# Kernel tuning notes

Measured on AMD Instinct MI355X. Metric: run time of the kernel, lower is better.

## Reference

```python
import jax, jax.numpy as jnp
import numpy as np

B, T, DM = 4, 2048, 2048
H, HKV, D = 16, 4, 128
ROPE_BASE = 10000.0


def setup_inputs() -> dict:
    key = jax.random.key(0)
    ks = jax.random.split(key, 5)
    x = jax.random.normal(ks[0], (B, T, DM), dtype=jnp.float32)
    s = 1.0 / np.sqrt(DM)
    Wq = jax.random.normal(ks[1], (H * D, DM), dtype=jnp.float32) * s
    Wk = jax.random.normal(ks[2], (HKV * D, DM), dtype=jnp.float32) * s
    Wv = jax.random.normal(ks[3], (HKV * D, DM), dtype=jnp.float32) * s
    Wo = jax.random.normal(ks[4], (DM, H * D), dtype=jnp.float32) * (1.0 / np.sqrt(H * D))
    temp = jnp.ones((H,), dtype=jnp.float32) * np.sqrt(D)  # registered buffer (unused on fallback path)
    return {"x": x, "Wq": Wq, "Wk": Wk, "Wv": Wv, "Wo": Wo, "temp": temp, "curvature": 1}


def _rms_norm(x):
    # F.rms_norm with default eps = finfo(dtype).eps, no learnable weight
    eps = jnp.finfo(x.dtype).eps
    return x * jax.lax.rsqrt(jnp.mean(x * x, axis=-1, keepdims=True) + eps)


def _rope_cos_sin(t_len, d, dtype):
    inv_freq = 1.0 / (ROPE_BASE ** (jnp.arange(0, d, 2, dtype=jnp.float32) / d))
    freqs = jnp.outer(jnp.arange(t_len, dtype=jnp.float32), inv_freq)  # [T, D/2]
    cos = jnp.cos(freqs)[None, :, None, :].astype(dtype)
    sin = jnp.sin(freqs)[None, :, None, :].astype(dtype)
    return cos, sin


def _apply_rotary(x, cos, sin):
    d = x.shape[-1] // 2
    x1, x2 = x[..., :d], x[..., d:]
    return jnp.concatenate([x1 * cos + x2 * sin, -x1 * sin + x2 * cos], axis=-1)


def reference(x, Wq, Wk, Wv, Wo, temp, curvature):
    b, t, _ = x.shape
    q = (x @ Wq.T).reshape(b, t, H, D)
    k = (x @ Wk.T).reshape(b, t, HKV, D)
    v = (x @ Wv.T).reshape(b, t, HKV, D)
    q, k = _rms_norm(q), _rms_norm(k)
    cos, sin = _rope_cos_sin(t, D, q.dtype)
    q = _apply_rotary(q, cos, sin)
    k = _apply_rotary(k, cos, sin)
    rep = H // HKV
    k = jnp.repeat(k, rep, axis=2)  # [b, t, H, D] GQA expand
    v = jnp.repeat(v, rep, axis=2)
    scale = 1.0 / np.sqrt(D)
    scores = jnp.einsum('bqhd,bkhd->bhqk', q, k) * scale
    causal = jnp.tril(jnp.ones((t, t), dtype=bool))
    scores = jnp.where(causal[None, None], scores, jnp.finfo(scores.dtype).min)
    p = jax.nn.softmax(scores, axis=-1)
    attn = jnp.einsum('bhqk,bkhd->bqhd', p, v).reshape(b, t, H * D)
    out = attn @ Wo.T
    spatial_norm = jnp.zeros((1,), dtype=x.dtype)
    return out, spatial_norm
```

## Files before the change

kernel.cpp:

```cpp
#include <hip/hip_runtime.h>
#include <hip/hip_bf16.h>

typedef __attribute__((ext_vector_type(8))) short short8;
typedef __attribute__((ext_vector_type(4))) float f32x4;
using bf16 = __hip_bfloat16;

__device__ inline unsigned short f2bfu(float x) {
  bf16 h = __float2bfloat16(x);
  return __builtin_bit_cast(unsigned short, h);
}

__device__ __forceinline__ void gll16(const void* g, void* l) {
  __builtin_amdgcn_global_load_lds(
      (const __attribute__((address_space(1))) unsigned int*)g,
      (__attribute__((address_space(3))) unsigned int*)l, 16, 0, 0);
}

__global__ __launch_bounds__(256) void cast_f32_bf16(const float4* __restrict__ src,
                                                     unsigned long long* __restrict__ dst,
                                                     int n4) {
  int i = blockIdx.x * 256 + threadIdx.x;
  if (i >= n4) return;
  float4 v = src[i];
  unsigned long long r = (unsigned long long)f2bfu(v.x)
                       | ((unsigned long long)f2bfu(v.y) << 16)
                       | ((unsigned long long)f2bfu(v.z) << 32)
                       | ((unsigned long long)f2bfu(v.w) << 48);
  dst[i] = r;
}

__device__ inline void store_cvt(float* p, float v) { *p = v; }
__device__ inline void store_cvt(bf16* p, float v) { *p = __float2bfloat16(v); }

template <typename OutT>
__global__ __launch_bounds__(256) void gemm_bt(const bf16* __restrict__ A,
                                               const bf16* __restrict__ B,
                                               OutT* __restrict__ C,
                                               int M, int N, int K) {
  __shared__ __align__(16) bf16 As[128][32];
  __shared__ __align__(16) bf16 Bs[128][32];
  const int tid = threadIdx.x;
  const int wave = tid >> 6, lane = tid & 63;
  const int wm = wave >> 1, wn = wave & 1;
  const int quad = lane >> 4, l16 = lane & 15;
  const int m0 = blockIdx.y * 128, n0 = blockIdx.x * 128;
  const int c0 = tid, c1 = tid + 256;
  const int r0 = c0 >> 2, k0 = (c0 & 3) * 8;
  const int r1 = c1 >> 2, k1 = (c1 & 3) * 8;
  f32x4 acc[4][4] = {};
  for (int kt = 0; kt < K; kt += 32) {
    gll16(&A[(size_t)(m0 + r0) * K + kt + k0], (bf16*)As + (size_t)c0 * 8);
    gll16(&A[(size_t)(m0 + r1) * K + kt + k1], (bf16*)As + (size_t)c1 * 8);
    gll16(&B[(size_t)(n0 + r0) * K + kt + k0], (bf16*)Bs + (size_t)c0 * 8);
    gll16(&B[(size_t)(n0 + r1) * K + kt + k1], (bf16*)Bs + (size_t)c1 * 8);
    __syncthreads();
    short8 af[4], bfr[4];
#pragma unroll
    for (int t = 0; t < 4; t++) {
      af[t]  = *(const short8*)&As[wm * 64 + t * 16 + l16][quad * 8];
      bfr[t] = *(const short8*)&Bs[wn * 64 + t * 16 + l16][quad * 8];
    }
#pragma unroll
    for (int im = 0; im < 4; im++)
#pragma unroll
      for (int in = 0; in < 4; in++)
        acc[im][in] = __builtin_amdgcn_mfma_f32_16x16x32_bf16(af[im], bfr[in], acc[im][in], 0, 0, 0);
    __syncthreads();
  }
#pragma unroll
  for (int im = 0; im < 4; im++)
#pragma unroll
    for (int in = 0; in < 4; in++) {
      int col = n0 + wn * 64 + in * 16 + l16;
#pragma unroll
      for (int r = 0; r < 4; r++) {
        int row = m0 + wm * 64 + im * 16 + quad * 4 + r;
        store_cvt(&C[(size_t)row * N + col], acc[im][in][r]);
      }
    }
}

__global__ __launch_bounds__(128) void norm_rope(const bf16* __restrict__ qkv,
                                                 bf16* __restrict__ qb,
                                                 bf16* __restrict__ kb,
                                                 bf16* __restrict__ vb) {
  const int token = blockIdx.y;
  const int slot = blockIdx.x;
  const int d = threadIdx.x;
  const int b = token >> 11, t = token & 2047;
  float val = __bfloat162float(qkv[(size_t)token * 3072 + slot * 128 + d]);
  if (slot >= 20) {
    vb[(((size_t)(b * 4 + (slot - 20))) * 2048 + t) * 128 + d] = __float2bfloat16(val);
    return;
  }
  float ss = val * val;
#pragma unroll
  for (int m = 1; m < 64; m <<= 1) ss += __shfl_xor(ss, m, 64);
  __shared__ float red[2];
  __shared__ float rowv[128];
  if ((threadIdx.x & 63) == 0) red[threadIdx.x >> 6] = ss;
  __syncthreads();
  float rinv = rsqrtf((red[0] + red[1]) * (1.0f / 128.0f) + 1.1920929e-7f);
  rowv[d] = val * rinv;
  __syncthreads();
  int i = d & 63;
  float x1 = rowv[i], x2 = rowv[i + 64];
  float inv_freq = __expf(-(float)i * (9.210340371976184f / 64.0f));
  float ph = (float)t * inv_freq;
  float c, s;
  __sincosf(ph, &s, &c);
  float outv = (d < 64) ? (x1 * c + x2 * s) : (x2 * c - x1 * s);
  if (slot < 16) {
    outv *= 0.08838834764831845f;
    qb[(((size_t)(b * 16 + slot)) * 2048 + t) * 128 + d] = __float2bfloat16(outv);
  } else {
    kb[(((size_t)(b * 4 + (slot - 16))) * 2048 + t) * 128 + d] = __float2bfloat16(outv);
  }
}

__global__ __launch_bounds__(256) void transpose_v(const bf16* __restrict__ vin,
                                                   bf16* __restrict__ vout) {
  __shared__ __align__(16) bf16 til[64][144];
  const int tid = threadIdx.x;
  const bf16* src = vin + ((size_t)blockIdx.y * 2048 + blockIdx.x * 64) * 128;
  bf16* dst = vout + (size_t)blockIdx.y * 128 * 2048 + blockIdx.x * 64;
#pragma unroll
  for (int p = 0; p < 4; p++) {
    int idx = p * 256 + tid;
    *(uint4*)&til[idx >> 4][(idx & 15) * 8] = *(const uint4*)&src[(size_t)(idx >> 4) * 128 + (idx & 15) * 8];
  }
  __syncthreads();
  const int ds = tid & 127;
  const int hs = tid >> 7;
#pragma unroll
  for (int p = 0; p < 4; p++) {
    int c8 = (p * 2 + hs) * 8;
    short8 v;
#pragma unroll
    for (int j = 0; j < 8; j++) v[j] = *(const short*)&til[c8 + j][ds];
    *(short8*)&dst[(size_t)ds * 2048 + c8] = v;
  }
}

__global__ __launch_bounds__(512, 4) void flash_attn(const bf16* __restrict__ qb,
                                                     const bf16* __restrict__ kb,
                                                     const bf16* __restrict__ vtg,
                                                     bf16* __restrict__ attnb) {
  const int qt = gridDim.x - 1 - blockIdx.x;
  const int bh = blockIdx.y;
  const int b = bh >> 4, h = bh & 15, hkv = h >> 2;
  const int q0 = qt * 128;
  const bf16* Q  = qb  + ((size_t)(b * 16 + h) * 2048 + q0) * 128;
  const bf16* Kp = kb  + (size_t)(b * 4 + hkv) * 2048 * 128;
  const bf16* Vg = vtg + (size_t)(b * 4 + hkv) * 128 * 2048;

  __shared__ __align__(16) bf16 Ks[64][136];
  __shared__ __align__(16) bf16 Vt[128][72];
  __shared__ __align__(16) bf16 Ps[8][16][72];

  const int tid = threadIdx.x;
  const int w = tid >> 6, lane = tid & 63;
  const int quad = lane >> 4, l16 = lane & 15;
  const int qw = q0 + w * 16;

  const int krow = tid >> 4, kc8 = (tid & 15) * 8;
  const int vrow = tid >> 3, vc8 = (tid & 7) * 8;

  short8 aq[4];
#pragma unroll
  for (int dk = 0; dk < 4; dk++)
    aq[dk] = *(const short8*)&Q[(size_t)(w * 16 + l16) * 128 + dk * 32 + quad * 8];

  f32x4 o[8] = {};
  float l_i[4] = {0.f, 0.f, 0.f, 0.f};

  const int ntiles = 2 * qt + 2;
  uint4 ka0 = *(const uint4*)&Kp[(size_t)krow * 128 + kc8];
  uint4 ka1 = *(const uint4*)&Kp[(size_t)(krow + 32) * 128 + kc8];
  uint4 va0 = *(const uint4*)&Vg[(size_t)vrow * 2048 + vc8];
  uint4 va1 = *(const uint4*)&Vg[(size_t)(vrow + 64) * 2048 + vc8];

  for (int kt = 0; kt < ntiles; kt++) {
    const int kv0 = kt * 64;
    *(uint4*)&Ks[krow][kc8]      = ka0;
    *(uint4*)&Ks[krow + 32][kc8] = ka1;
    *(uint4*)&Vt[vrow][vc8]      = va0;
    *(uint4*)&Vt[vrow + 64][vc8] = va1;
    __syncthreads();

    const int nkv0 = min(kv0 + 64, (ntiles - 1) * 64);
    ka0 = *(const uint4*)&Kp[(size_t)(nkv0 + krow) * 128 + kc8];
    ka1 = *(const uint4*)&Kp[(size_t)(nkv0 + krow + 32) * 128 + kc8];
    va0 = *(const uint4*)&Vg[(size_t)vrow * 2048 + nkv0 + vc8];
    va1 = *(const uint4*)&Vg[(size_t)(vrow + 64) * 2048 + nkv0 + vc8];

    if (kv0 <= qw + 15) {
      f32x4 s[4] = {};
#pragma unroll
      for (int nt = 0; nt < 4; nt++)
#pragma unroll
        for (int dk = 0; dk < 4; dk++) {
          short8 bk = *(const short8*)&Ks[nt * 16 + l16][dk * 32 + quad * 8];
          s[nt] = __builtin_amdgcn_mfma_f32_16x16x32_bf16(aq[dk], bk, s[nt], 0, 0, 0);
        }

      const bool dtile = (kv0 + 63 > qw);
      const int qrow = qw + quad * 4;
#pragma unroll
      for (int nt = 0; nt < 4; nt++) {
        const int kcol = kv0 + nt * 16 + l16;
#pragma unroll
        for (int r = 0; r < 4; r++) {
          float p = __expf(s[nt][r] - 12.0f);
          if (dtile && kcol > qrow + r) p = 0.f;
          l_i[r] += p;
          Ps[w][quad * 4 + r][nt * 16 + l16] = __float2bfloat16(p);
        }
      }
      __threadfence_block();

      short8 ap[2];
#pragma unroll
      for (int kk = 0; kk < 2; kk++)
        ap[kk] = *(const short8*)&Ps[w][l16][kk * 32 + quad * 8];
#pragma unroll
      for (int vt = 0; vt < 8; vt++)
#pragma unroll
        for (int kk = 0; kk < 2; kk++) {
          short8 bv = *(const short8*)&Vt[vt * 16 + l16][kk * 32 + quad * 8];
          o[vt] = __builtin_amdgcn_mfma_f32_16x16x32_bf16(ap[kk], bv, o[vt], 0, 0, 0);
        }
    }
    __syncthreads();
  }

#pragma unroll
  for (int r = 0; r < 4; r++) {
#pragma unroll
    for (int mm = 1; mm < 16; mm <<= 1) l_i[r] += __shfl_xor(l_i[r], mm, 64);
  }
#pragma unroll
  for (int r = 0; r < 4; r++) {
    float inv = 1.0f / l_i[r];
    int trow = qw + quad * 4 + r;
    size_t base = ((size_t)b * 2048 + trow) * 2048 + h * 128;
#pragma unroll
    for (int vt = 0; vt < 8; vt++)
      attnb[base + vt * 16 + l16] = __float2bfloat16(o[vt][r] * inv);
  }
}

__global__ void finalize(float* out) {
  if (threadIdx.x == 0 && blockIdx.x == 0) out[(size_t)8192 * 2048] = 0.0f;
}

extern "C" void kernel_launch(void* const* d_in, const int* in_sizes, int n_in,
                              void* d_out, int out_size, void* d_ws, size_t ws_size,
                              hipStream_t stream) {
  const float* x  = (const float*)d_in[0];
  const float* Wq = (const float*)d_in[1];
  const float* Wk = (const float*)d_in[2];
  const float* Wv = (const float*)d_in[3];
  const float* Wo = (const float*)d_in[4];
  float* out = (float*)d_out;

  char* ws = (char*)d_ws;
  bf16* xb    = (bf16*)(ws);
  bf16* wqkv  = (bf16*)(ws + 33554432);
  bf16* vtb   = (bf16*)(ws + 33554432);
  bf16* wob   = (bf16*)(ws + 46137344);
  bf16* qkvb  = (bf16*)(ws + 54525952);
  bf16* qb    = (bf16*)(ws + 104857600);
  bf16* kb    = (bf16*)(ws + 138412032);
  bf16* vb    = (bf16*)(ws + 146800640);
  bf16* attnb = qkvb;

  cast_f32_bf16<<<16384, 256, 0, stream>>>((const float4*)x,  (unsigned long long*)xb, 4194304);
  cast_f32_bf16<<<4096,  256, 0, stream>>>((const float4*)Wq, (unsigned long long*)wqkv, 1048576);
  cast_f32_bf16<<<1024,  256, 0, stream>>>((const float4*)Wk, (unsigned long long*)(wqkv + 2048 * 2048), 262144);
  cast_f32_bf16<<<1024,  256, 0, stream>>>((const float4*)Wv, (unsigned long long*)(wqkv + 2560 * 2048), 262144);
  cast_f32_bf16<<<4096,  256, 0, stream>>>((const float4*)Wo, (unsigned long long*)wob, 1048576);

  gemm_bt<bf16><<<dim3(24, 64), 256, 0, stream>>>(xb, wqkv, qkvb, 8192, 3072, 2048);
  norm_rope<<<dim3(24, 8192), 128, 0, stream>>>(qkvb, qb, kb, vb);
  transpose_v<<<dim3(32, 16), 256, 0, stream>>>(vb, vtb);
  flash_attn<<<dim3(16, 64), 512, 0, stream>>>(qb, kb, vtb, attnb);
  gemm_bt<float><<<dim3(16, 64), 256, 0, stream>>>(attnb, wob, out, 8192, 2048, 2048);
  finalize<<<1, 64, 0, stream>>>(out);
}
```

Baseline: 628.4 us.

## Rework norm_rope to wave-per-row, read V directly, pair causal attention tiles

The norm_rope kernel now uses one wavefront per 128-wide head row in a grid-stride loop, replacing one 128-thread block per row and slot. This removes shared-memory reductions and block syncs. The V copy pass is dropped, and transpose_v reads V straight from the fused QKV buffer. Flash attention launches 512 blocks, and each block handles a long and a short causal query tile (item and 1023-item) to balance work across blocks. The cost is fewer resident blocks and sequential processing of the two items within a block.

```diff
diff --git a/kernel.cpp b/kernel.cpp
--- a/kernel.cpp
+++ b/kernel.cpp
@@ -80,54 +80,54 @@
     }
 }
 
-__global__ __launch_bounds__(128) void norm_rope(const bf16* __restrict__ qkv,
+__global__ __launch_bounds__(256) void norm_rope(const bf16* __restrict__ qkv,
                                                  bf16* __restrict__ qb,
-                                                 bf16* __restrict__ kb,
-                                                 bf16* __restrict__ vb) {
-  const int token = blockIdx.y;
-  const int slot = blockIdx.x;
-  const int d = threadIdx.x;
-  const int b = token >> 11, t = token & 2047;
-  float val = __bfloat162float(qkv[(size_t)token * 3072 + slot * 128 + d]);
-  if (slot >= 20) {
-    vb[(((size_t)(b * 4 + (slot - 20))) * 2048 + t) * 128 + d] = __float2bfloat16(val);
-    return;
-  }
-  float ss = val * val;
-#pragma unroll
-  for (int m = 1; m < 64; m <<= 1) ss += __shfl_xor(ss, m, 64);
-  __shared__ float red[2];
-  __shared__ float rowv[128];
-  if ((threadIdx.x & 63) == 0) red[threadIdx.x >> 6] = ss;
-  __syncthreads();
-  float rinv = rsqrtf((red[0] + red[1]) * (1.0f / 128.0f) + 1.1920929e-7f);
-  rowv[d] = val * rinv;
-  __syncthreads();
-  int i = d & 63;
-  float x1 = rowv[i], x2 = rowv[i + 64];
-  float inv_freq = __expf(-(float)i * (9.210340371976184f / 64.0f));
-  float ph = (float)t * inv_freq;
-  float c, s;
-  __sincosf(ph, &s, &c);
-  float outv = (d < 64) ? (x1 * c + x2 * s) : (x2 * c - x1 * s);
-  if (slot < 16) {
-    outv *= 0.08838834764831845f;
-    qb[(((size_t)(b * 16 + slot)) * 2048 + t) * 128 + d] = __float2bfloat16(outv);
-  } else {
-    kb[(((size_t)(b * 4 + (slot - 16))) * 2048 + t) * 128 + d] = __float2bfloat16(outv);
-  }
-}
-
-__global__ __launch_bounds__(256) void transpose_v(const bf16* __restrict__ vin,
+                                                 bf16* __restrict__ kb) {
+  const int lane = threadIdx.x & 63;
+  const int gw = (blockIdx.x * 256 + threadIdx.x) >> 6;
+  const int nw = (gridDim.x * 256) >> 6;
+  const float inv_freq = __expf(-(float)lane * (9.210340371976184f / 64.0f));
+  for (int row = gw; row < 20 * 8192; row += nw) {
+    const int slot = row >> 13, token = row & 8191;
+    const int b = token >> 11, t = token & 2047;
+    const bf16* src = qkv + (size_t)token * 3072 + slot * 128;
+    float x1 = __bfloat162float(src[lane]);
+    float x2 = __bfloat162float(src[lane + 64]);
+    float ss = x1 * x1 + x2 * x2;
+#pragma unroll
+    for (int m = 1; m < 64; m <<= 1) ss += __shfl_xor(ss, m, 64);
+    float rinv = rsqrtf(ss * (1.0f / 128.0f) + 1.1920929e-7f);
+    x1 *= rinv; x2 *= rinv;
+    float c, s;
+    __sincosf((float)t * inv_freq, &s, &c);
+    float o1 = x1 * c + x2 * s;
+    float o2 = x2 * c - x1 * s;
+    bf16* dst;
+    if (slot < 16) {
+      o1 *= 0.08838834764831845f;
+      o2 *= 0.08838834764831845f;
+      dst = qb + (((size_t)(b * 16 + slot)) * 2048 + t) * 128;
+    } else {
+      dst = kb + (((size_t)(b * 4 + (slot - 16))) * 2048 + t) * 128;
+    }
+    dst[lane] = __float2bfloat16(o1);
+    dst[lane + 64] = __float2bfloat16(o2);
+  }
+}
+
+__global__ __launch_bounds__(256) void transpose_v(const bf16* __restrict__ qkv,
                                                    bf16* __restrict__ vout) {
   __shared__ __align__(16) bf16 til[64][144];
   const int tid = threadIdx.x;
-  const bf16* src = vin + ((size_t)blockIdx.y * 2048 + blockIdx.x * 64) * 128;
-  bf16* dst = vout + (size_t)blockIdx.y * 128 * 2048 + blockIdx.x * 64;
+  const int s = blockIdx.y;
+  const int b = s >> 2, hkv = s & 3;
+  const bf16* src = qkv + ((size_t)(b * 2048 + blockIdx.x * 64)) * 3072 + 2560 + hkv * 128;
+  bf16* dst = vout + (size_t)s * 128 * 2048 + blockIdx.x * 64;
 #pragma unroll
   for (int p = 0; p < 4; p++) {
     int idx = p * 256 + tid;
-    *(uint4*)&til[idx >> 4][(idx & 15) * 8] = *(const uint4*)&src[(size_t)(idx >> 4) * 128 + (idx & 15) * 8];
+    *(uint4*)&til[idx >> 4][(idx & 15) * 8] =
+        *(const uint4*)&src[(size_t)(idx >> 4) * 3072 + (idx & 15) * 8];
   }
   __syncthreads();
   const int ds = tid & 127;
@@ -146,14 +146,6 @@
                                                      const bf16* __restrict__ kb,
                                                      const bf16* __restrict__ vtg,
                                                      bf16* __restrict__ attnb) {
-  const int qt = gridDim.x - 1 - blockIdx.x;
-  const int bh = blockIdx.y;
-  const int b = bh >> 4, h = bh & 15, hkv = h >> 2;
-  const int q0 = qt * 128;
-  const bf16* Q  = qb  + ((size_t)(b * 16 + h) * 2048 + q0) * 128;
-  const bf16* Kp = kb  + (size_t)(b * 4 + hkv) * 2048 * 128;
-  const bf16* Vg = vtg + (size_t)(b * 4 + hkv) * 128 * 2048;
-
   __shared__ __align__(16) bf16 Ks[64][136];
   __shared__ __align__(16) bf16 Vt[128][72];
   __shared__ __align__(16) bf16 Ps[8][16][72];
@@ -161,92 +153,101 @@
   const int tid = threadIdx.x;
   const int w = tid >> 6, lane = tid & 63;
   const int quad = lane >> 4, l16 = lane & 15;
-  const int qw = q0 + w * 16;
-
   const int krow = tid >> 4, kc8 = (tid & 15) * 8;
   const int vrow = tid >> 3, vc8 = (tid & 7) * 8;
 
-  short8 aq[4];
-#pragma unroll
-  for (int dk = 0; dk < 4; dk++)
-    aq[dk] = *(const short8*)&Q[(size_t)(w * 16 + l16) * 128 + dk * 32 + quad * 8];
-
-  f32x4 o[8] = {};
-  float l_i[4] = {0.f, 0.f, 0.f, 0.f};
-
-  const int ntiles = 2 * qt + 2;
-  uint4 ka0 = *(const uint4*)&Kp[(size_t)krow * 128 + kc8];
-  uint4 ka1 = *(const uint4*)&Kp[(size_t)(krow + 32) * 128 + kc8];
-  uint4 va0 = *(const uint4*)&Vg[(size_t)vrow * 2048 + vc8];
-  uint4 va1 = *(const uint4*)&Vg[(size_t)(vrow + 64) * 2048 + vc8];
-
-  for (int kt = 0; kt < ntiles; kt++) {
-    const int kv0 = kt * 64;
-    *(uint4*)&Ks[krow][kc8]      = ka0;
-    *(uint4*)&Ks[krow + 32][kc8] = ka1;
-    *(uint4*)&Vt[vrow][vc8]      = va0;
-    *(uint4*)&Vt[vrow + 64][vc8] = va1;
-    __syncthreads();
-
-    const int nkv0 = min(kv0 + 64, (ntiles - 1) * 64);
-    ka0 = *(const uint4*)&Kp[(size_t)(nkv0 + krow) * 128 + kc8];
-    ka1 = *(const uint4*)&Kp[(size_t)(nkv0 + krow + 32) * 128 + kc8];
-    va0 = *(const uint4*)&Vg[(size_t)vrow * 2048 + nkv0 + vc8];
-    va1 = *(const uint4*)&Vg[(size_t)(vrow + 64) * 2048 + nkv0 + vc8];
-
-    if (kv0 <= qw + 15) {
-      f32x4 s[4] = {};
-#pragma unroll
-      for (int nt = 0; nt < 4; nt++)
-#pragma unroll
-        for (int dk = 0; dk < 4; dk++) {
-          short8 bk = *(const short8*)&Ks[nt * 16 + l16][dk * 32 + quad * 8];
-          s[nt] = __builtin_amdgcn_mfma_f32_16x16x32_bf16(aq[dk], bk, s[nt], 0, 0, 0);
+  for (int it = 0; it < 2; it++) {
+    const int item = it == 0 ? blockIdx.x : 1023 - blockIdx.x;
+    const int qt = item >> 6, bh = item & 63;
+    const int b = bh >> 4, h = bh & 15, hkv = h >> 2;
+    const int q0 = qt * 128;
+    const bf16* Q  = qb  + ((size_t)(b * 16 + h) * 2048 + q0) * 128;
+    const bf16* Kp = kb  + (size_t)(b * 4 + hkv) * 2048 * 128;
+    const bf16* Vg = vtg + (size_t)(b * 4 + hkv) * 128 * 2048;
+    const int qw = q0 + w * 16;
+
+    short8 aq[4];
+#pragma unroll
+    for (int dk = 0; dk < 4; dk++)
+      aq[dk] = *(const short8*)&Q[(size_t)(w * 16 + l16) * 128 + dk * 32 + quad * 8];
+
+    f32x4 o[8] = {};
+    float l_i[4] = {0.f, 0.f, 0.f, 0.f};
+
+    const int ntiles = 2 * qt + 2;
+    uint4 ka0 = *(const uint4*)&Kp[(size_t)krow * 128 + kc8];
+    uint4 ka1 = *(const uint4*)&Kp[(size_t)(krow + 32) * 128 + kc8];
+    uint4 va0 = *(const uint4*)&Vg[(size_t)vrow * 2048 + vc8];
+    uint4 va1 = *(const uint4*)&Vg[(size_t)(vrow + 64) * 2048 + vc8];
+
+    for (int kt = 0; kt < ntiles; kt++) {
+      const int kv0 = kt * 64;
+      *(uint4*)&Ks[krow][kc8]      = ka0;
+      *(uint4*)&Ks[krow + 32][kc8] = ka1;
+      *(uint4*)&Vt[vrow][vc8]      = va0;
+      *(uint4*)&Vt[vrow + 64][vc8] = va1;
+      __syncthreads();
+
+      const int nkv0 = min(kv0 + 64, (ntiles - 1) * 64);
+      ka0 = *(const uint4*)&Kp[(size_t)(nkv0 + krow) * 128 + kc8];
+      ka1 = *(const uint4*)&Kp[(size_t)(nkv0 + krow + 32) * 128 + kc8];
+      va0 = *(const uint4*)&Vg[(size_t)vrow * 2048 + nkv0 + vc8];
+      va1 = *(const uint4*)&Vg[(size_t)(vrow + 64) * 2048 + nkv0 + vc8];
+
+      if (kv0 <= qw + 15) {
+        f32x4 s[4] = {};
+#pragma unroll
+        for (int nt = 0; nt < 4; nt++)
+#pragma unroll
+          for (int dk = 0; dk < 4; dk++) {
+            short8 bk = *(const short8*)&Ks[nt * 16 + l16][dk * 32 + quad * 8];
+            s[nt] = __builtin_amdgcn_mfma_f32_16x16x32_bf16(aq[dk], bk, s[nt], 0, 0, 0);
+          }
+
+        const bool dtile = (kv0 + 63 > qw);
+        const int qrow = qw + quad * 4;
+#pragma unroll
+        for (int nt = 0; nt < 4; nt++) {
+          const int kcol = kv0 + nt * 16 + l16;
+#pragma unroll
+          for (int r = 0; r < 4; r++) {
+            float p = __expf(s[nt][r] - 12.0f);
+            if (dtile && kcol > qrow + r) p = 0.f;
+            l_i[r] += p;
+            Ps[w][quad * 4 + r][nt * 16 + l16] = __float2bfloat16(p);
+          }
         }
-
-      const bool dtile = (kv0 + 63 > qw);
-      const int qrow = qw + quad * 4;
-#pragma unroll
-      for (int nt = 0; nt < 4; nt++) {
-        const int kcol = kv0 + nt * 16 + l16;
-#pragma unroll
-        for (int r = 0; r < 4; r++) {
-          float p = __expf(s[nt][r] - 12.0f);
-          if (dtile && kcol > qrow + r) p = 0.f;
-          l_i[r] += p;
-          Ps[w][quad * 4 + r][nt * 16 + l16] = __float2bfloat16(p);
-        }
+        __threadfence_block();
+
+        short8 ap[2];
+#pragma unroll
+        for (int kk = 0; kk < 2; kk++)
+          ap[kk] = *(const short8*)&Ps[w][l16][kk * 32 + quad * 8];
+#pragma unroll
+        for (int vt = 0; vt < 8; vt++)
+#pragma unroll
+          for (int kk = 0; kk < 2; kk++) {
+            short8 bv = *(const short8*)&Vt[vt * 16 + l16][kk * 32 + quad * 8];
+            o[vt] = __builtin_amdgcn_mfma_f32_16x16x32_bf16(ap[kk], bv, o[vt], 0, 0, 0);
+          }
       }
-      __threadfence_block();
-
-      short8 ap[2];
-#pragma unroll
-      for (int kk = 0; kk < 2; kk++)
-        ap[kk] = *(const short8*)&Ps[w][l16][kk * 32 + quad * 8];
+      __syncthreads();
+    }
+
+#pragma unroll
+    for (int r = 0; r < 4; r++) {
+#pragma unroll
+      for (int mm = 1; mm < 16; mm <<= 1) l_i[r] += __shfl_xor(l_i[r], mm, 64);
+    }
+#pragma unroll
+    for (int r = 0; r < 4; r++) {
+      float inv = 1.0f / l_i[r];
+      int trow = qw + quad * 4 + r;
+      size_t base = ((size_t)b * 2048 + trow) * 2048 + h * 128;
 #pragma unroll
       for (int vt = 0; vt < 8; vt++)
-#pragma unroll
-        for (int kk = 0; kk < 2; kk++) {
-          short8 bv = *(const short8*)&Vt[vt * 16 + l16][kk * 32 + quad * 8];
-          o[vt] = __builtin_amdgcn_mfma_f32_16x16x32_bf16(ap[kk], bv, o[vt], 0, 0, 0);
-        }
-    }
-    __syncthreads();
-  }
-
-#pragma unroll
-  for (int r = 0; r < 4; r++) {
-#pragma unroll
-    for (int mm = 1; mm < 16; mm <<= 1) l_i[r] += __shfl_xor(l_i[r], mm, 64);
-  }
-#pragma unroll
-  for (int r = 0; r < 4; r++) {
-    float inv = 1.0f / l_i[r];
-    int trow = qw + quad * 4 + r;
-    size_t base = ((size_t)b * 2048 + trow) * 2048 + h * 128;
-#pragma unroll
-    for (int vt = 0; vt < 8; vt++)
-      attnb[base + vt * 16 + l16] = __float2bfloat16(o[vt][r] * inv);
+        attnb[base + vt * 16 + l16] = __float2bfloat16(o[vt][r] * inv);
+    }
   }
 }
 
@@ -272,7 +273,6 @@
   bf16* qkvb  = (bf16*)(ws + 54525952);
   bf16* qb    = (bf16*)(ws + 104857600);
   bf16* kb    = (bf16*)(ws + 138412032);
-  bf16* vb    = (bf16*)(ws + 146800640);
   bf16* attnb = qkvb;
 
   cast_f32_bf16<<<16384, 256, 0, stream>>>((const float4*)x,  (unsigned long long*)xb, 4194304);
@@ -282,9 +282,9 @@
   cast_f32_bf16<<<4096,  256, 0, stream>>>((const float4*)Wo, (unsigned long long*)wob, 1048576);
 
   gemm_bt<bf16><<<dim3(24, 64), 256, 0, stream>>>(xb, wqkv, qkvb, 8192, 3072, 2048);
-  norm_rope<<<dim3(24, 8192), 128, 0, stream>>>(qkvb, qb, kb, vb);
-  transpose_v<<<dim3(32, 16), 256, 0, stream>>>(vb, vtb);
-  flash_attn<<<dim3(16, 64), 512, 0, stream>>>(qb, kb, vtb, attnb);
+  norm_rope<<<4096, 256, 0, stream>>>(qkvb, qb, kb);
+  transpose_v<<<dim3(32, 16), 256, 0, stream>>>(qkvb, vtb);
+  flash_attn<<<512, 512, 0, stream>>>(qb, kb, vtb, attnb);
   gemm_bt<float><<<dim3(16, 64), 256, 0, stream>>>(attnb, wob, out, 8192, 2048, 2048);
   finalize<<<1, 64, 0, stream>>>(out);
 }
```

Result: faster. 537.9 us (-14.4%).
